# Kernel optimization log

Measured on AMD Instinct MI355X. Metric: run time of the kernel, lower is better.

Reference implementation:

```python
import jax, jax.numpy as jnp
import numpy as np

N = 8192
EMB = 256
KDIM = 32
AR = 1024
UTYPE = 233
TEMP = 0.8


def setup_inputs() -> dict:
    key = jax.random.key(0)
    ks = jax.random.split(key, 16)
    s = 0.05
    f32 = jnp.float32
    inp = {
        'utype_mask': jax.random.uniform(ks[0], (UTYPE,), f32),
        'entity_mask': jnp.ones((N,), f32),
        'entity_encodings': jax.random.normal(ks[1], (N, EMB), f32),
        'autoregressive_encoding': jax.random.normal(ks[2], (AR,), f32),
        # func_embed: Linear(233,256)+ReLU
        'W_fe': jax.random.normal(ks[3], (EMB, UTYPE), f32) * s, 'b_fe': jnp.zeros((EMB,), f32),
        # entity_keys: Conv1d(256,32,1) == pointwise linear
        'W_k': jax.random.normal(ks[4], (KDIM, EMB), f32) * s, 'b_k': jnp.zeros((KDIM,), f32),
        # argenc[0]: Linear(1024,256)
        'W_a0': jax.random.normal(ks[5], (EMB, AR), f32) * s, 'b_a0': jnp.zeros((EMB,), f32),
        # argenc[1]: ReLU -> Linear(256,32) -> ReLU
        'W_a1': jax.random.normal(ks[6], (KDIM, EMB), f32) * s, 'b_a1': jnp.zeros((KDIM,), f32),
        # LSTM(64,32) gates (forget, input-sigmoid, input-tanh, output) + shared LayerNorm(32)
        'W_f': jax.random.normal(ks[7], (KDIM, 2 * KDIM), f32) * s, 'b_f': jnp.zeros((KDIM,), f32),
        'W_i0': jax.random.normal(ks[8], (KDIM, 2 * KDIM), f32) * s, 'b_i0': jnp.zeros((KDIM,), f32),
        'W_i1': jax.random.normal(ks[9], (KDIM, 2 * KDIM), f32) * s, 'b_i1': jnp.zeros((KDIM,), f32),
        'W_o': jax.random.normal(ks[10], (KDIM, 2 * KDIM), f32) * s, 'b_o': jnp.zeros((KDIM,), f32),
        'ln_g': jnp.ones((KDIM,), f32), 'ln_b': jnp.zeros((KDIM,), f32),
        # argenc[3]: Linear(32,1024)+ReLU
        'W_a3': jax.random.normal(ks[11], (AR, KDIM), f32) * s, 'b_a3': jnp.zeros((AR,), f32),
        'self_unit_ct': 64,
    }
    return inp


def reference(utype_mask, entity_mask, entity_encodings, autoregressive_encoding,
              W_fe, b_fe, W_k, b_k, W_a0, b_a0, W_a1, b_a1,
              W_f, b_f, W_i0, b_i0, W_i1, b_i1, W_o, b_o, ln_g, ln_b,
              W_a3, b_a3, self_unit_ct):
    n = entity_encodings.shape[0]
    steps = min(64, int(self_unit_ct))

    def ln(x):  # shared LayerNorm(32), torch eps=1e-5, biased var
        m = x.mean()
        v = ((x - m) ** 2).mean()
        return (x - m) * jax.lax.rsqrt(v + 1e-5) * ln_g + ln_b

    def lstm(x, h):
        forget = ln(jax.nn.sigmoid(W_f @ x + b_f))
        remember = ln(jax.nn.sigmoid(W_i0 @ x + b_i0) * jnp.tanh(W_i1 @ x + b_i1))
        new_h = remember + forget * h
        out = jnp.tanh(new_h) * ln(jax.nn.sigmoid(W_o @ x + b_o))
        return out, new_h

    func_embed = jax.nn.relu(W_fe @ utype_mask + b_fe)          # (256,)
    keys = W_k @ entity_encodings.T + b_k[:, None]               # (32, N)

    def step(carry, _):
        q, h, mask, ar, sel, done = carry
        active = jnp.logical_not(done)
        i0 = W_a0 @ ar + b_a0 + func_embed                       # (256,)
        i1 = jax.nn.relu(W_a1 @ jax.nn.relu(i0) + b_a1)          # (32,)
        qn, hn = lstm(jnp.concatenate([i1, q]), h)
        sig = jax.nn.sigmoid(qn @ keys)                          # (N,)
        v = jnp.nan_to_num(jnp.exp(jnp.log(sig) / TEMP))
        ssum = v.sum()
        valid = ssum != 0
        soft = jnp.where(valid, v / jnp.where(valid, ssum, 1.0), 0.0)
        row = jnp.where(active & valid, soft, 0.0)
        pick = jnp.argmax(soft)                                  # deterministic stand-in for multinomial sample
        hit = active & valid & (mask[pick] != 0)
        selection = keys[:, pick]
        centered = selection - selection.mean()
        nan_free = jnp.logical_not(jnp.any(jnp.isnan(centered)))
        mask = jnp.where(hit, mask.at[pick].set(0.0), mask)
        sel = jnp.where(hit, sel.at[pick].set(1.0), sel)
        ar = jnp.where(hit & nan_free, ar + jax.nn.relu(W_a3 @ centered + b_a3), ar)
        done = done | (hit & jnp.logical_not(nan_free))          # emulates break
        q = jnp.where(active, qn, q)
        h = jnp.where(active, hn, h)
        return (q, h, mask, ar, sel, done), row

    init = (jnp.zeros((KDIM,), jnp.float32), jnp.zeros((KDIM,), jnp.float32),
            entity_mask, autoregressive_encoding,
            jnp.zeros((n,), jnp.float32), jnp.array(False))
    (_, _, _, ar_out, sel_out, _), rows = jax.lax.scan(step, init, None, length=steps)
    unit_logits = jnp.zeros((n, n), jnp.float32).at[:steps].set(rows)
    return unit_logits, sel_out, ar_out
```

## Files before the change

### kernel.cpp

```cpp
#include <hip/hip_runtime.h>
#include <math.h>


typedef float v4f __attribute__((ext_vector_type(4)));
typedef unsigned long long ull;

#define N_ENT 8192
#define EMB   256
#define KD    32
#define ARD   1024
#define UT    233
#define NSCAN 32
#define NZERO 224
#define NBLK  256

#define WS_KEYS 0
#define WS_C0   262144
#define WS_PAIR 262400
#define PR_RI0W  0
#define PR_CRI0  512
#define PR_CPART 577
#define PR_KMAX  641
#define PR_SACC  705
#define NPAIRS   737

struct Params {
  const float *um, *emask, *enc, *arin, *W_fe, *b_fe, *W_k, *b_k,
              *W_a0, *b_a0, *W_a1, *b_a1, *W_f, *b_f, *W_i0, *b_i0,
              *W_i1, *b_i1, *W_o, *b_o, *ln_g, *ln_b, *W_a3, *b_a3;
  const int* ct;
  float* out;
  float* wsf;
  int*   wsi;
};

__device__ __forceinline__ ull ld_pair(ull* p_) {
  return __hip_atomic_load(p_, __ATOMIC_RELAXED, __HIP_MEMORY_SCOPE_AGENT);
}
__device__ __forceinline__ void st_pair(ull* p_, ull v) {
  __hip_atomic_store(p_, v, __ATOMIC_RELAXED, __HIP_MEMORY_SCOPE_AGENT);
}
__device__ __forceinline__ void wait_ctr(ull* c, ull target) {
  int guard = 0;
  while (__hip_atomic_load(c, __ATOMIC_RELAXED, __HIP_MEMORY_SCOPE_AGENT) < target) {
    __builtin_amdgcn_s_sleep(1);
    if (++guard > (1 << 20)) break;
  }
}

__global__ __launch_bounds__(256) void k_init(Params p) {
  __shared__ float enc_s[32 * 260];
  __shared__ float um_s[UT];
  const int tid = threadIdx.x, bid = blockIdx.x;
  float* keys = p.wsf + WS_KEYS;

  if (bid == 0 && tid < UT) um_s[tid] = p.um[tid];
  if (bid == 3) {
    ull* pr = (ull*)(p.wsf + WS_PAIR);
    for (int i = tid; i < NPAIRS; i += 256) pr[i] = 0ull;
  }

  const int j0 = bid * 32;
  #pragma unroll
  for (int i = 0; i < 8; ++i) {
    int idx = i * 256 + tid;
    int row = idx >> 6, c4 = idx & 63;
    v4f v = *(const v4f*)(p.enc + (size_t)(j0 + row) * EMB + c4 * 4);
    *(v4f*)&enc_s[row * 260 + c4 * 4] = v;
  }
  __syncthreads();
  {
    const int jl = tid >> 3, kg = tid & 7;
    float acc[4];
    #pragma unroll
    for (int kk = 0; kk < 4; ++kk) acc[kk] = p.b_k[kg * 4 + kk];
    for (int e4 = 0; e4 < 64; ++e4) {
      v4f x = *(const v4f*)&enc_s[jl * 260 + e4 * 4];
      #pragma unroll
      for (int kk = 0; kk < 4; ++kk) {
        v4f w = *(const v4f*)(p.W_k + (size_t)(kg * 4 + kk) * EMB + e4 * 4);
        acc[kk] += x.x * w.x + x.y * w.y + x.z * w.z + x.w * w.w;
      }
    }
    const int j = j0 + jl;
    #pragma unroll
    for (int kk = 0; kk < 4; ++kk) keys[(size_t)(kg * 4 + kk) * N_ENT + j] = acc[kk];
  }
  if (bid == 0) {
    float a = p.b_fe[tid];
    const float* wr = p.W_fe + (size_t)tid * UT;
    for (int u = 0; u < UT; ++u) a += wr[u] * um_s[u];
    p.wsf[WS_C0 + tid] = fmaxf(a, 0.f) + p.b_a0[tid];
  }
}

__global__ __launch_bounds__(256, 1) void k_scan(Params p) {
  const int tid = threadIdx.x, bid = blockIdx.x;
  int ctv = p.ct[0];
  const int steps = ctv < 0 ? 0 : (ctv > 64 ? 64 : ctv);
  const size_t NN = (size_t)N_ENT * N_ENT;

  if (bid >= NSCAN) {
    v4f z = (v4f){0.f, 0.f, 0.f, 0.f};
    v4f* o4 = (v4f*)p.out;
    const size_t tot = NN / 4;
    for (size_t i = (size_t)steps * (N_ENT / 4) + (size_t)(bid - NSCAN) * 256 + tid;
         i < tot; i += (size_t)NZERO * 256)
      __builtin_nontemporal_store(z, o4 + i);
    return;
  }

  __shared__ float ar_s[32 * 33];
  __shared__ float ri0_s[8 * 33];
  __shared__ unsigned maskb[256], selb[256];
  __shared__ float x_i1[32], q_s[32], h_s[32], qnf[32];
  __shared__ float garr[128], fog[32], rem[32], og[32], cent[32];
  __shared__ float b_a1s[32], gb_s[128], lng_s[32], lnb_s[32], c0own[8];
  __shared__ float reds[4], rmaxs[4];
  __shared__ int   ridxs[4];
  __shared__ float ssum_s;
  __shared__ int   upd_s, done_s;

  ull*   pairb = (ull*)(p.wsf + WS_PAIR);
  ull*   ri0w  = pairb + PR_RI0W;
  ull*   cri0  = pairb + PR_CRI0;
  ull*   cpart = pairb + PR_CPART;
  ull*   kmaxp = pairb + PR_KMAX;
  float* saccp = (float*)(pairb + PR_SACC);
  const float* keys = p.wsf + WS_KEYS;

  for (int i = tid; i < ARD; i += 256) ar_s[(i >> 5) * 33 + (i & 31)] = p.arin[i];
  {
    unsigned mb = 0u;
    const float* em = p.emask + (size_t)tid * 32;
    #pragma unroll
    for (int j = 0; j < 32; ++j) mb |= (em[j] != 0.f) ? (1u << j) : 0u;
    maskb[tid] = mb; selb[tid] = 0u;
  }
  if (tid < 32) {
    b_a1s[tid] = p.b_a1[tid];
    lng_s[tid] = p.ln_g[tid]; lnb_s[tid] = p.ln_b[tid];
    q_s[tid] = 0.f; h_s[tid] = 0.f; qnf[tid] = 0.f; x_i1[tid] = 0.f;
  }
  if (tid < 128) {
    const int g = tid >> 5, r = tid & 31;
    const float* bg = (g == 0) ? p.b_f : (g == 1) ? p.b_i0 : (g == 2) ? p.b_i1 : p.b_o;
    gb_s[tid] = bg[r];
  }
  if (tid < 8) c0own[tid] = p.wsf[WS_C0 + bid * 8 + tid];
  if (tid == 0) done_s = 0;

  v4f w0[8];
  { const float* s = p.W_a0 + (size_t)(bid * 8 + (tid >> 5)) * ARD + (tid & 31) * 32;
    #pragma unroll
    for (int i = 0; i < 8; ++i) w0[i] = ((const v4f*)s)[i]; }
  v4f w1[8];
  { const float* s = p.W_a1 + (size_t)(tid >> 3) * EMB + (tid & 7) * 32;
    #pragma unroll
    for (int i = 0; i < 8; ++i) w1[i] = ((const v4f*)s)[i]; }
  v4f wg[8];
  { const int rowg = tid >> 1, g = rowg >> 5, r = rowg & 31, half = tid & 1;
    const float* W = (g == 0) ? p.W_f : (g == 1) ? p.W_i0 : (g == 2) ? p.W_i1 : p.W_o;
    const float* s = W + r * 64 + half * 32;
    #pragma unroll
    for (int i = 0; i < 8; ++i) wg[i] = ((const v4f*)s)[i]; }
  float kc[32];
  { const int gcol = bid * 256 + tid;
    #pragma unroll
    for (int k = 0; k < 32; ++k) kc[k] = keys[(size_t)k * N_ENT + gcol]; }
  __syncthreads();

  auto produce = [&](int tt) {
    const int seg = tid & 31, rl = tid >> 5;
    const float* a = &ar_s[seg * 33];
    float pa = 0.f;
    #pragma unroll
    for (int i = 0; i < 8; ++i) {
      v4f av = *(const v4f*)(a + 4 * i);
      pa += w0[i].x * av.x + w0[i].y * av.y + w0[i].z * av.z + w0[i].w * av.w;
    }
    #pragma unroll
    for (int m = 16; m; m >>= 1) pa += __shfl_xor(pa, m);
    if (seg == 0)
      st_pair(&ri0w[(tt & 1) * 256 + bid * 8 + rl],
              (ull)__float_as_uint(fmaxf(pa + c0own[rl], 0.f)));
  };
  produce(0);
  __syncthreads();
  if (tid == 0)
    __hip_atomic_fetch_add(&cri0[0], 1ull, __ATOMIC_RELAXED, __HIP_MEMORY_SCOPE_AGENT);

  float v_reg = 0.f;
  for (int t = 0; t < steps; ++t) {
    if (tid == 0) wait_ctr(&cri0[t], (ull)NSCAN);
    __syncthreads();
    {
      ull u = ld_pair(&ri0w[(t & 1) * 256 + tid]);
      ri0_s[(tid >> 5) * 33 + (tid & 31)] = __uint_as_float((unsigned)u);
    }
    __syncthreads();
    const int act = (done_s == 0);
    {
      const int r = tid >> 3, s8 = tid & 7;
      float p1 = 0.f;
      #pragma unroll
      for (int i = 0; i < 8; ++i) {
        const float* xx = &ri0_s[s8 * 33 + 4 * i];
        p1 += w1[i].x * xx[0] + w1[i].y * xx[1] + w1[i].z * xx[2] + w1[i].w * xx[3];
      }
      #pragma unroll
      for (int m = 4; m; m >>= 1) p1 += __shfl_xor(p1, m);
      if (s8 == 0) x_i1[r] = fmaxf(p1 + b_a1s[r], 0.f);
    }
    __syncthreads();
    {
      const int rowg = tid >> 1, g = rowg >> 5, half = tid & 1;
      const float* xsrc = half ? q_s : x_i1;
      float pg = 0.f;
      #pragma unroll
      for (int i = 0; i < 8; ++i)
        pg += wg[i].x * xsrc[4 * i] + wg[i].y * xsrc[4 * i + 1] +
              wg[i].z * xsrc[4 * i + 2] + wg[i].w * xsrc[4 * i + 3];
      pg += __shfl_xor(pg, 1);
      if (!half) {
        pg += gb_s[rowg];
        garr[rowg] = (g == 2) ? tanhf(pg) : 1.f / (1.f + __expf(-pg));
      }
    }
    __syncthreads();
    {
      const int w = tid >> 6, k = tid & 63;
      if (w < 3 && k < 32) {
        float a = (w == 0) ? garr[k] : (w == 1) ? garr[32 + k] * garr[64 + k] : garr[96 + k];
        float s = a;
        #pragma unroll
        for (int m = 16; m; m >>= 1) s += __shfl_xor(s, m);
        const float mean = s * (1.f / 32.f);
        const float d = a - mean;
        float vv = d * d;
        #pragma unroll
        for (int m = 16; m; m >>= 1) vv += __shfl_xor(vv, m);
        vv *= (1.f / 32.f);
        const float y = d * rsqrtf(vv + 1e-5f) * lng_s[k] + lnb_s[k];
        if (w == 0) fog[k] = y; else if (w == 1) rem[k] = y; else og[k] = y;
      }
    }
    __syncthreads();
    if (tid < 32) {
      const float nh = rem[tid] + fog[tid] * h_s[tid];
      const float qv = tanhf(nh) * og[tid];
      qnf[tid] = qv;
      if (act) { h_s[tid] = nh; q_s[tid] = qv; }
    }
    __syncthreads();

    {
      float dot = 0.f;
      #pragma unroll
      for (int k = 0; k < 32; ++k) dot += qnf[k] * kc[k];
      const float sig = 1.f / (1.f + __expf(-dot));
      const float v = __expf(__logf(sig) / 0.8f);
      v_reg = v;
      float sv = v, mv = v;
      int mi = (bid << 8) + tid;
      #pragma unroll
      for (int m = 32; m; m >>= 1) {
        sv += __shfl_xor(sv, m);
        const float ov = __shfl_xor(mv, m);
        const int oi = __shfl_xor(mi, m);
        if (ov > mv || (ov == mv && oi < mi)) { mv = ov; mi = oi; }
      }
      const int wv = tid >> 6;
      if ((tid & 63) == 0) { reds[wv] = sv; rmaxs[wv] = mv; ridxs[wv] = mi; }
    }
    __syncthreads();
    if (tid == 0) {
      float Sb = ((reds[0] + reds[1]) + reds[2]) + reds[3];
      float Mb = rmaxs[0]; int Ib = ridxs[0];
      #pragma unroll
      for (int i2 = 1; i2 < 4; ++i2)
        if (rmaxs[i2] > Mb || (rmaxs[i2] == Mb && ridxs[i2] < Ib)) { Mb = rmaxs[i2]; Ib = ridxs[i2]; }
      __hip_atomic_fetch_add(&saccp[t], Sb, __ATOMIC_RELAXED, __HIP_MEMORY_SCOPE_AGENT);
      const ull key = ((ull)__float_as_uint(Mb) << 32) | (ull)(0xFFFFFFFFu - (unsigned)Ib);
      __hip_atomic_fetch_max(&kmaxp[t], key, __ATOMIC_RELAXED, __HIP_MEMORY_SCOPE_AGENT);
      asm volatile("s_waitcnt vmcnt(0)" ::: "memory");
      __hip_atomic_fetch_add(&cpart[t], 1ull, __ATOMIC_RELAXED, __HIP_MEMORY_SCOPE_AGENT);
    }

    if (tid == 0) wait_ctr(&cpart[t], (ull)NSCAN);
    __syncthreads();
    if (tid < 32) {
      const float s = __hip_atomic_load(&saccp[t], __ATOMIC_RELAXED, __HIP_MEMORY_SCOPE_AGENT);
      const ull km = ld_pair(&kmaxp[t]);
      const int ii = (int)(0xFFFFFFFFu - (unsigned)(km & 0xFFFFFFFFull));
      const float kv = keys[(size_t)tid * N_ENT + ii];
      float mn = kv;
      #pragma unroll
      for (int mm = 16; mm; mm >>= 1) mn += __shfl_xor(mn, mm);
      mn *= (1.f / 32.f);
      const float cv = kv - mn;
      cent[tid] = cv;
      const unsigned long long bb = __ballot(cv != cv);
      if (tid == 0) {
        const int valid = (s != 0.f);
        const int nf = (bb == 0) ? 1 : 0;
        const unsigned mw = maskb[ii >> 5];
        const int hit = (act && valid && ((mw >> (ii & 31)) & 1)) ? 1 : 0;
        ssum_s = s;
        upd_s = (hit && nf) ? 1 : 0;
        if (hit) {
          maskb[ii >> 5] = mw & ~(1u << (ii & 31));
          selb[ii >> 5] |= (1u << (ii & 31));
          if (!nf) done_s = 1;
        }
      }
    }
    __syncthreads();
    {
      const float S = ssum_s;
      const float rowv = (act && (S != 0.f)) ? (v_reg / S) : 0.f;
      __builtin_nontemporal_store(rowv, p.out + (size_t)t * N_ENT + (bid << 8) + tid);
    }
    if (upd_s) {
      #pragma unroll
      for (int rr = 0; rr < 4; ++rr) {
        const int r = tid + rr * 256;
        const float* wr = p.W_a3 + (size_t)r * KD;
        float dl = p.b_a3[r];
        #pragma unroll
        for (int c4 = 0; c4 < 8; ++c4) {
          v4f wv4 = *(const v4f*)(wr + 4 * c4);
          dl += wv4.x * cent[4 * c4] + wv4.y * cent[4 * c4 + 1] +
                wv4.z * cent[4 * c4 + 2] + wv4.w * cent[4 * c4 + 3];
        }
        if (dl > 0.f) ar_s[(r >> 5) * 33 + (r & 31)] += dl;
      }
    }
    __syncthreads();
    produce(t + 1);
    __syncthreads();
    if (tid == 0)
      __hip_atomic_fetch_add(&cri0[t + 1], 1ull, __ATOMIC_RELAXED, __HIP_MEMORY_SCOPE_AGENT);
  }
  __syncthreads();

  if (bid == 0) {
    for (int i = tid; i < N_ENT; i += 256)
      p.out[NN + i] = ((selb[i >> 5] >> (i & 31)) & 1u) ? 1.f : 0.f;
  } else if (bid == 1) {
    for (int i = tid; i < ARD; i += 256)
      p.out[NN + N_ENT + i] = ar_s[(i >> 5) * 33 + (i & 31)];
  }
}

extern "C" void kernel_launch(void* const* d_in, const int* in_sizes, int n_in,
                              void* d_out, int out_size, void* d_ws, size_t ws_size,
                              hipStream_t stream) {
  (void)in_sizes; (void)n_in; (void)out_size; (void)ws_size;
  Params p;
  p.um    = (const float*)d_in[0];
  p.emask = (const float*)d_in[1];
  p.enc   = (const float*)d_in[2];
  p.arin  = (const float*)d_in[3];
  p.W_fe  = (const float*)d_in[4];
  p.b_fe  = (const float*)d_in[5];
  p.W_k   = (const float*)d_in[6];
  p.b_k   = (const float*)d_in[7];
  p.W_a0  = (const float*)d_in[8];
  p.b_a0  = (const float*)d_in[9];
  p.W_a1  = (const float*)d_in[10];
  p.b_a1  = (const float*)d_in[11];
  p.W_f   = (const float*)d_in[12];
  p.b_f   = (const float*)d_in[13];
  p.W_i0  = (const float*)d_in[14];
  p.b_i0  = (const float*)d_in[15];
  p.W_i1  = (const float*)d_in[16];
  p.b_i1  = (const float*)d_in[17];
  p.W_o   = (const float*)d_in[18];
  p.b_o   = (const float*)d_in[19];
  p.ln_g  = (const float*)d_in[20];
  p.ln_b  = (const float*)d_in[21];
  p.W_a3  = (const float*)d_in[22];
  p.b_a3  = (const float*)d_in[23];
  p.ct    = (const int*)d_in[24];
  p.out   = (float*)d_out;
  p.wsf   = (float*)d_ws;
  p.wsi   = (int*)d_ws;

  hipLaunchKernelGGL(k_init, dim3(NBLK), dim3(256), 0, stream, p);
  hipLaunchKernelGGL(k_scan, dim3(NBLK), dim3(256), 0, stream, p);
}
```

Baseline: 881.1 us.

## Shorten the per-step critical path with a single wavefront for AR update and produce

```diff
diff --git a/kernel.cpp b/kernel.cpp
--- a/kernel.cpp
+++ b/kernel.cpp
@@ -48,6 +48,10 @@
   }
 }
 
+__device__ __forceinline__ void bar_lds() {
+  asm volatile("s_waitcnt lgkmcnt(0)\n\ts_barrier" ::: "memory");
+}
+
 __global__ __launch_bounds__(256) void k_init(Params p) {
   __shared__ float enc_s[32 * 260];
   __shared__ float um_s[UT];
@@ -110,6 +114,7 @@
     return;
   }
 
+  __shared__ float wa0_lds[32 * 64 * 4];
   __shared__ float ar_s[32 * 33];
   __shared__ float ri0_s[8 * 33];
   __shared__ unsigned maskb[256], selb[256];
@@ -118,8 +123,7 @@
   __shared__ float b_a1s[32], gb_s[128], lng_s[32], lnb_s[32], c0own[8];
   __shared__ float reds[4], rmaxs[4];
   __shared__ int   ridxs[4];
-  __shared__ float ssum_s;
-  __shared__ int   upd_s, done_s;
+  __shared__ int   done_s;
 
   ull*   pairb = (ull*)(p.wsf + WS_PAIR);
   ull*   ri0w  = pairb + PR_RI0W;
@@ -130,6 +134,11 @@
   const float* keys = p.wsf + WS_KEYS;
 
   for (int i = tid; i < ARD; i += 256) ar_s[(i >> 5) * 33 + (i & 31)] = p.arin[i];
+  for (int e = tid; e < 8 * ARD; e += 256) {
+    const int r = e >> 10, c = e & 1023;
+    const int seg = c >> 7, rem2 = c & 127, i = rem2 >> 2, j = rem2 & 3;
+    wa0_lds[(i * 64 + seg * 8 + r) * 4 + j] = p.W_a0[(size_t)(bid * 8 + r) * ARD + c];
+  }
   {
     unsigned mb = 0u;
     const float* em = p.emask + (size_t)tid * 32;
@@ -150,10 +159,6 @@
   if (tid < 8) c0own[tid] = p.wsf[WS_C0 + bid * 8 + tid];
   if (tid == 0) done_s = 0;
 
-  v4f w0[8];
-  { const float* s = p.W_a0 + (size_t)(bid * 8 + (tid >> 5)) * ARD + (tid & 31) * 32;
-    #pragma unroll
-    for (int i = 0; i < 8; ++i) w0[i] = ((const v4f*)s)[i]; }
   v4f w1[8];
   { const float* s = p.W_a1 + (size_t)(tid >> 3) * EMB + (tid & 7) * 32;
     #pragma unroll
@@ -171,34 +176,37 @@
   __syncthreads();
 
   auto produce = [&](int tt) {
-    const int seg = tid & 31, rl = tid >> 5;
-    const float* a = &ar_s[seg * 33];
+    const int r = tid >> 3, seg = tid & 7;
     float pa = 0.f;
     #pragma unroll
-    for (int i = 0; i < 8; ++i) {
-      v4f av = *(const v4f*)(a + 4 * i);
-      pa += w0[i].x * av.x + w0[i].y * av.y + w0[i].z * av.z + w0[i].w * av.w;
-    }
-    #pragma unroll
-    for (int m = 16; m; m >>= 1) pa += __shfl_xor(pa, m);
+    for (int i = 0; i < 32; ++i) {
+      v4f wv = *(const v4f*)&wa0_lds[(i * 64 + seg * 8 + r) * 4];
+      const int c = seg * 128 + 4 * i;
+      const float* av = &ar_s[(c >> 5) * 33 + (c & 31)];
+      pa += wv.x * av[0] + wv.y * av[1] + wv.z * av[2] + wv.w * av[3];
+    }
+    pa += __shfl_xor(pa, 1);
+    pa += __shfl_xor(pa, 2);
+    pa += __shfl_xor(pa, 4);
     if (seg == 0)
-      st_pair(&ri0w[(tt & 1) * 256 + bid * 8 + rl],
-              (ull)__float_as_uint(fmaxf(pa + c0own[rl], 0.f)));
+      st_pair(&ri0w[(tt & 1) * 256 + bid * 8 + r],
+              (ull)__float_as_uint(fmaxf(pa + c0own[r], 0.f)));
   };
-  produce(0);
-  __syncthreads();
-  if (tid == 0)
-    __hip_atomic_fetch_add(&cri0[0], 1ull, __ATOMIC_RELAXED, __HIP_MEMORY_SCOPE_AGENT);
+  if (tid < 64) {
+    produce(0);
+    asm volatile("s_waitcnt vmcnt(0)" ::: "memory");
+    if (tid == 0)
+      __hip_atomic_fetch_add(&cri0[0], 1ull, __ATOMIC_RELAXED, __HIP_MEMORY_SCOPE_AGENT);
+  }
 
   float v_reg = 0.f;
   for (int t = 0; t < steps; ++t) {
-    if (tid == 0) wait_ctr(&cri0[t], (ull)NSCAN);
-    __syncthreads();
+    wait_ctr(&cri0[t], (ull)NSCAN);
     {
       ull u = ld_pair(&ri0w[(t & 1) * 256 + tid]);
       ri0_s[(tid >> 5) * 33 + (tid & 31)] = __uint_as_float((unsigned)u);
     }
-    __syncthreads();
+    bar_lds();
     const int act = (done_s == 0);
     {
       const int r = tid >> 3, s8 = tid & 7;
@@ -212,7 +220,7 @@
       for (int m = 4; m; m >>= 1) p1 += __shfl_xor(p1, m);
       if (s8 == 0) x_i1[r] = fmaxf(p1 + b_a1s[r], 0.f);
     }
-    __syncthreads();
+    bar_lds();
     {
       const int rowg = tid >> 1, g = rowg >> 5, half = tid & 1;
       const float* xsrc = half ? q_s : x_i1;
@@ -227,7 +235,7 @@
         garr[rowg] = (g == 2) ? tanhf(pg) : 1.f / (1.f + __expf(-pg));
       }
     }
-    __syncthreads();
+    bar_lds();
     {
       const int w = tid >> 6, k = tid & 63;
       if (w < 3 && k < 32) {
@@ -245,14 +253,14 @@
         if (w == 0) fog[k] = y; else if (w == 1) rem[k] = y; else og[k] = y;
       }
     }
-    __syncthreads();
+    bar_lds();
     if (tid < 32) {
       const float nh = rem[tid] + fog[tid] * h_s[tid];
       const float qv = tanhf(nh) * og[tid];
       qnf[tid] = qv;
       if (act) { h_s[tid] = nh; q_s[tid] = qv; }
     }
-    __syncthreads();
+    bar_lds();
 
     {
       float dot = 0.f;
@@ -273,7 +281,7 @@
       const int wv = tid >> 6;
       if ((tid & 63) == 0) { reds[wv] = sv; rmaxs[wv] = mv; ridxs[wv] = mi; }
     }
-    __syncthreads();
+    bar_lds();
     if (tid == 0) {
       float Sb = ((reds[0] + reds[1]) + reds[2]) + reds[3];
       float Mb = rmaxs[0]; int Ib = ridxs[0];
@@ -287,60 +295,61 @@
       __hip_atomic_fetch_add(&cpart[t], 1ull, __ATOMIC_RELAXED, __HIP_MEMORY_SCOPE_AGENT);
     }
 
-    if (tid == 0) wait_ctr(&cpart[t], (ull)NSCAN);
-    __syncthreads();
-    if (tid < 32) {
-      const float s = __hip_atomic_load(&saccp[t], __ATOMIC_RELAXED, __HIP_MEMORY_SCOPE_AGENT);
-      const ull km = ld_pair(&kmaxp[t]);
-      const int ii = (int)(0xFFFFFFFFu - (unsigned)(km & 0xFFFFFFFFull));
-      const float kv = keys[(size_t)tid * N_ENT + ii];
-      float mn = kv;
-      #pragma unroll
-      for (int mm = 16; mm; mm >>= 1) mn += __shfl_xor(mn, mm);
-      mn *= (1.f / 32.f);
-      const float cv = kv - mn;
-      cent[tid] = cv;
-      const unsigned long long bb = __ballot(cv != cv);
-      if (tid == 0) {
-        const int valid = (s != 0.f);
-        const int nf = (bb == 0) ? 1 : 0;
-        const unsigned mw = maskb[ii >> 5];
-        const int hit = (act && valid && ((mw >> (ii & 31)) & 1)) ? 1 : 0;
-        ssum_s = s;
-        upd_s = (hit && nf) ? 1 : 0;
-        if (hit) {
-          maskb[ii >> 5] = mw & ~(1u << (ii & 31));
-          selb[ii >> 5] |= (1u << (ii & 31));
-          if (!nf) done_s = 1;
+    wait_ctr(&cpart[t], (ull)NSCAN);
+    const float S = __hip_atomic_load(&saccp[t], __ATOMIC_RELAXED, __HIP_MEMORY_SCOPE_AGENT);
+    const ull km = ld_pair(&kmaxp[t]);
+    const int ii = (int)(0xFFFFFFFFu - (unsigned)(km & 0xFFFFFFFFull));
+    const int valid = (S != 0.f) ? 1 : 0;
+    const float rowv = (act && valid) ? (v_reg / S) : 0.f;
+    if (tid >= 64) {
+      __builtin_nontemporal_store(rowv, p.out + (size_t)t * N_ENT + (bid << 8) + tid);
+    } else {
+      if (tid < 32) {
+        const float kv = keys[(size_t)tid * N_ENT + ii];
+        float mn = kv;
+        #pragma unroll
+        for (int mm = 16; mm; mm >>= 1) mn += __shfl_xor(mn, mm);
+        mn *= (1.f / 32.f);
+        cent[tid] = kv - mn;
+      }
+      asm volatile("s_waitcnt lgkmcnt(0)" ::: "memory");
+      const unsigned mw = maskb[ii >> 5];
+      float cw[32]; int nanf = 0;
+      #pragma unroll
+      for (int g2 = 0; g2 < 8; ++g2) {
+        v4f x = *(const v4f*)&cent[4 * g2];
+        cw[4 * g2] = x.x; cw[4 * g2 + 1] = x.y; cw[4 * g2 + 2] = x.z; cw[4 * g2 + 3] = x.w;
+        nanf |= (x.x != x.x) | (x.y != x.y) | (x.z != x.z) | (x.w != x.w);
+      }
+      const int hit = (act && valid && ((mw >> (ii & 31)) & 1)) ? 1 : 0;
+      const int upd = (hit && !nanf) ? 1 : 0;
+      if (upd) {
+        #pragma unroll
+        for (int k = 0; k < 16; ++k) {
+          const int r = tid + 64 * k;
+          const float* wr = p.W_a3 + (size_t)r * KD;
+          float dl = p.b_a3[r];
+          #pragma unroll
+          for (int c4 = 0; c4 < 8; ++c4) {
+            v4f wv4 = *(const v4f*)(wr + 4 * c4);
+            dl += wv4.x * cw[4 * c4] + wv4.y * cw[4 * c4 + 1] +
+                  wv4.z * cw[4 * c4 + 2] + wv4.w * cw[4 * c4 + 3];
+          }
+          if (dl > 0.f) ar_s[(r >> 5) * 33 + (r & 31)] += dl;
         }
       }
-    }
-    __syncthreads();
-    {
-      const float S = ssum_s;
-      const float rowv = (act && (S != 0.f)) ? (v_reg / S) : 0.f;
+      if (tid == 0 && hit) {
+        maskb[ii >> 5] = mw & ~(1u << (ii & 31));
+        selb[ii >> 5] |= (1u << (ii & 31));
+        if (nanf) done_s = 1;
+      }
+      asm volatile("s_waitcnt lgkmcnt(0)" ::: "memory");
+      produce(t + 1);
+      asm volatile("s_waitcnt vmcnt(0)" ::: "memory");
+      if (tid == 0)
+        __hip_atomic_fetch_add(&cri0[t + 1], 1ull, __ATOMIC_RELAXED, __HIP_MEMORY_SCOPE_AGENT);
       __builtin_nontemporal_store(rowv, p.out + (size_t)t * N_ENT + (bid << 8) + tid);
     }
-    if (upd_s) {
-      #pragma unroll
-      for (int rr = 0; rr < 4; ++rr) {
-        const int r = tid + rr * 256;
-        const float* wr = p.W_a3 + (size_t)r * KD;
-        float dl = p.b_a3[r];
-        #pragma unroll
-        for (int c4 = 0; c4 < 8; ++c4) {
-          v4f wv4 = *(const v4f*)(wr + 4 * c4);
-          dl += wv4.x * cent[4 * c4] + wv4.y * cent[4 * c4 + 1] +
-                wv4.z * cent[4 * c4 + 2] + wv4.w * cent[4 * c4 + 3];
-        }
-        if (dl > 0.f) ar_s[(r >> 5) * 33 + (r & 31)] += dl;
-      }
-    }
-    __syncthreads();
-    produce(t + 1);
-    __syncthreads();
-    if (tid == 0)
-      __hip_atomic_fetch_add(&cri0[t + 1], 1ull, __ATOMIC_RELAXED, __HIP_MEMORY_SCOPE_AGENT);
   }
   __syncthreads();
 
```

Measured after the change: 1.025 ms. 16.3% more time.

## Recompute full W_a0 matvec redundantly per block to drop one grid barrier per step

Applied to the files above, without the earlier changes.

```diff
diff --git a/kernel.cpp b/kernel.cpp
--- a/kernel.cpp
+++ b/kernel.cpp
@@ -17,12 +17,10 @@
 #define WS_KEYS 0
 #define WS_C0   262144
 #define WS_PAIR 262400
-#define PR_RI0W  0
-#define PR_CRI0  512
-#define PR_CPART 577
-#define PR_KMAX  641
-#define PR_SACC  705
-#define NPAIRS   737
+#define PR_CPART 0
+#define PR_KMAX  64
+#define PR_SACC  128
+#define NPAIRS   160
 
 struct Params {
   const float *um, *emask, *enc, *arin, *W_fe, *b_fe, *W_k, *b_k,
@@ -37,9 +35,6 @@
 __device__ __forceinline__ ull ld_pair(ull* p_) {
   return __hip_atomic_load(p_, __ATOMIC_RELAXED, __HIP_MEMORY_SCOPE_AGENT);
 }
-__device__ __forceinline__ void st_pair(ull* p_, ull v) {
-  __hip_atomic_store(p_, v, __ATOMIC_RELAXED, __HIP_MEMORY_SCOPE_AGENT);
-}
 __device__ __forceinline__ void wait_ctr(ull* c, ull target) {
   int guard = 0;
   while (__hip_atomic_load(c, __ATOMIC_RELAXED, __HIP_MEMORY_SCOPE_AGENT) < target) {
@@ -112,24 +107,24 @@
 
   __shared__ float ar_s[32 * 33];
   __shared__ float ri0_s[8 * 33];
+  __shared__ float c0_s[256];
   __shared__ unsigned maskb[256], selb[256];
   __shared__ float x_i1[32], q_s[32], h_s[32], qnf[32];
   __shared__ float garr[128], fog[32], rem[32], og[32], cent[32];
-  __shared__ float b_a1s[32], gb_s[128], lng_s[32], lnb_s[32], c0own[8];
+  __shared__ float b_a1s[32], gb_s[128], lng_s[32], lnb_s[32];
   __shared__ float reds[4], rmaxs[4];
   __shared__ int   ridxs[4];
   __shared__ float ssum_s;
   __shared__ int   upd_s, done_s;
 
   ull*   pairb = (ull*)(p.wsf + WS_PAIR);
-  ull*   ri0w  = pairb + PR_RI0W;
-  ull*   cri0  = pairb + PR_CRI0;
   ull*   cpart = pairb + PR_CPART;
   ull*   kmaxp = pairb + PR_KMAX;
   float* saccp = (float*)(pairb + PR_SACC);
   const float* keys = p.wsf + WS_KEYS;
 
   for (int i = tid; i < ARD; i += 256) ar_s[(i >> 5) * 33 + (i & 31)] = p.arin[i];
+  c0_s[tid] = p.wsf[WS_C0 + tid];
   {
     unsigned mb = 0u;
     const float* em = p.emask + (size_t)tid * 32;
@@ -147,13 +142,8 @@
     const float* bg = (g == 0) ? p.b_f : (g == 1) ? p.b_i0 : (g == 2) ? p.b_i1 : p.b_o;
     gb_s[tid] = bg[r];
   }
-  if (tid < 8) c0own[tid] = p.wsf[WS_C0 + bid * 8 + tid];
   if (tid == 0) done_s = 0;
 
-  v4f w0[8];
-  { const float* s = p.W_a0 + (size_t)(bid * 8 + (tid >> 5)) * ARD + (tid & 31) * 32;
-    #pragma unroll
-    for (int i = 0; i < 8; ++i) w0[i] = ((const v4f*)s)[i]; }
   v4f w1[8];
   { const float* s = p.W_a1 + (size_t)(tid >> 3) * EMB + (tid & 7) * 32;
     #pragma unroll
@@ -170,36 +160,38 @@
     for (int k = 0; k < 32; ++k) kc[k] = keys[(size_t)k * N_ENT + gcol]; }
   __syncthreads();
 
-  auto produce = [&](int tt) {
-    const int seg = tid & 31, rl = tid >> 5;
-    const float* a = &ar_s[seg * 33];
-    float pa = 0.f;
-    #pragma unroll
-    for (int i = 0; i < 8; ++i) {
-      v4f av = *(const v4f*)(a + 4 * i);
-      pa += w0[i].x * av.x + w0[i].y * av.y + w0[i].z * av.z + w0[i].w * av.w;
-    }
-    #pragma unroll
-    for (int m = 16; m; m >>= 1) pa += __shfl_xor(pa, m);
-    if (seg == 0)
-      st_pair(&ri0w[(tt & 1) * 256 + bid * 8 + rl],
-              (ull)__float_as_uint(fmaxf(pa + c0own[rl], 0.f)));
+  auto recompute_ri0 = [&]() {
+    const int seg = tid & 7, r0 = tid >> 3;
+    v4f arseg[32];
+    #pragma unroll
+    for (int i = 0; i < 32; ++i) {
+      const int c = seg * 128 + 4 * i;
+      const float* a = &ar_s[(c >> 5) * 33 + (c & 31)];
+      arseg[i] = (v4f){a[0], a[1], a[2], a[3]};
+    }
+    #pragma unroll
+    for (int pass = 0; pass < 8; ++pass) {
+      const int r = r0 + 32 * pass;
+      const float* wrow = p.W_a0 + (size_t)r * ARD + seg * 128;
+      float pa = 0.f;
+      #pragma unroll
+      for (int i = 0; i < 32; ++i) {
+        v4f wv = ((const v4f*)wrow)[i];
+        pa += wv.x * arseg[i].x + wv.y * arseg[i].y + wv.z * arseg[i].z + wv.w * arseg[i].w;
+      }
+      pa += __shfl_xor(pa, 1);
+      pa += __shfl_xor(pa, 2);
+      pa += __shfl_xor(pa, 4);
+      if (seg == 0) ri0_s[(r >> 5) * 33 + (r & 31)] = fmaxf(pa + c0_s[r], 0.f);
+    }
   };
-  produce(0);
+  recompute_ri0();
   __syncthreads();
-  if (tid == 0)
-    __hip_atomic_fetch_add(&cri0[0], 1ull, __ATOMIC_RELAXED, __HIP_MEMORY_SCOPE_AGENT);
 
   float v_reg = 0.f;
   for (int t = 0; t < steps; ++t) {
-    if (tid == 0) wait_ctr(&cri0[t], (ull)NSCAN);
-    __syncthreads();
-    {
-      ull u = ld_pair(&ri0w[(t & 1) * 256 + tid]);
-      ri0_s[(tid >> 5) * 33 + (tid & 31)] = __uint_as_float((unsigned)u);
-    }
-    __syncthreads();
     const int act = (done_s == 0);
+
     {
       const int r = tid >> 3, s8 = tid & 7;
       float p1 = 0.f;
@@ -285,10 +277,10 @@
       __hip_atomic_fetch_max(&kmaxp[t], key, __ATOMIC_RELAXED, __HIP_MEMORY_SCOPE_AGENT);
       asm volatile("s_waitcnt vmcnt(0)" ::: "memory");
       __hip_atomic_fetch_add(&cpart[t], 1ull, __ATOMIC_RELAXED, __HIP_MEMORY_SCOPE_AGENT);
-    }
-
-    if (tid == 0) wait_ctr(&cpart[t], (ull)NSCAN);
-    __syncthreads();
+      wait_ctr(&cpart[t], (ull)NSCAN);
+    }
+    __syncthreads();
+
     if (tid < 32) {
       const float s = __hip_atomic_load(&saccp[t], __ATOMIC_RELAXED, __HIP_MEMORY_SCOPE_AGENT);
       const ull km = ld_pair(&kmaxp[t]);
@@ -337,10 +329,8 @@
       }
     }
     __syncthreads();
-    produce(t + 1);
-    __syncthreads();
-    if (tid == 0)
-      __hip_atomic_fetch_add(&cri0[t + 1], 1ull, __ATOMIC_RELAXED, __HIP_MEMORY_SCOPE_AGENT);
+    recompute_ri0();
+    __syncthreads();
   }
   __syncthreads();
 
```

Result: slower. 2.670 ms (+203.0%).

## Halve scan blocks so each handles 512 entities and 16 W_a0 rows

Applied to the files above, without the earlier changes.

```diff
diff --git a/kernel.cpp b/kernel.cpp
--- a/kernel.cpp
+++ b/kernel.cpp
@@ -10,8 +10,8 @@
 #define KD    32
 #define ARD   1024
 #define UT    233
-#define NSCAN 32
-#define NZERO 224
+#define NSCAN 16
+#define NZERO 240
 #define NBLK  256
 
 #define WS_KEYS 0
@@ -115,7 +115,7 @@
   __shared__ unsigned maskb[256], selb[256];
   __shared__ float x_i1[32], q_s[32], h_s[32], qnf[32];
   __shared__ float garr[128], fog[32], rem[32], og[32], cent[32];
-  __shared__ float b_a1s[32], gb_s[128], lng_s[32], lnb_s[32], c0own[8];
+  __shared__ float b_a1s[32], gb_s[128], lng_s[32], lnb_s[32], c0own[16];
   __shared__ float reds[4], rmaxs[4];
   __shared__ int   ridxs[4];
   __shared__ float ssum_s;
@@ -147,13 +147,13 @@
     const float* bg = (g == 0) ? p.b_f : (g == 1) ? p.b_i0 : (g == 2) ? p.b_i1 : p.b_o;
     gb_s[tid] = bg[r];
   }
-  if (tid < 8) c0own[tid] = p.wsf[WS_C0 + bid * 8 + tid];
+  if (tid < 16) c0own[tid] = p.wsf[WS_C0 + bid * 16 + tid];
   if (tid == 0) done_s = 0;
 
-  v4f w0[8];
-  { const float* s = p.W_a0 + (size_t)(bid * 8 + (tid >> 5)) * ARD + (tid & 31) * 32;
-    #pragma unroll
-    for (int i = 0; i < 8; ++i) w0[i] = ((const v4f*)s)[i]; }
+  v4f w0[16];
+  { const float* s = p.W_a0 + (size_t)(bid * 16 + (tid >> 4)) * ARD + (tid & 15) * 64;
+    #pragma unroll
+    for (int i = 0; i < 16; ++i) w0[i] = ((const v4f*)s)[i]; }
   v4f w1[8];
   { const float* s = p.W_a1 + (size_t)(tid >> 3) * EMB + (tid & 7) * 32;
     #pragma unroll
@@ -164,33 +164,38 @@
     const float* s = W + r * 64 + half * 32;
     #pragma unroll
     for (int i = 0; i < 8; ++i) wg[i] = ((const v4f*)s)[i]; }
-  float kc[32];
-  { const int gcol = bid * 256 + tid;
-    #pragma unroll
-    for (int k = 0; k < 32; ++k) kc[k] = keys[(size_t)k * N_ENT + gcol]; }
+  float kc0[32], kc1[32];
+  { const int g0 = bid * 512 + tid, g1 = g0 + 256;
+    #pragma unroll
+    for (int k = 0; k < 32; ++k) {
+      kc0[k] = keys[(size_t)k * N_ENT + g0];
+      kc1[k] = keys[(size_t)k * N_ENT + g1];
+    } }
   __syncthreads();
 
   auto produce = [&](int tt) {
-    const int seg = tid & 31, rl = tid >> 5;
-    const float* a = &ar_s[seg * 33];
+    const int r = tid >> 4, seg = tid & 15;
     float pa = 0.f;
     #pragma unroll
-    for (int i = 0; i < 8; ++i) {
-      v4f av = *(const v4f*)(a + 4 * i);
-      pa += w0[i].x * av.x + w0[i].y * av.y + w0[i].z * av.z + w0[i].w * av.w;
-    }
-    #pragma unroll
-    for (int m = 16; m; m >>= 1) pa += __shfl_xor(pa, m);
+    for (int i = 0; i < 16; ++i) {
+      const int c = seg * 64 + 4 * i;
+      const float* a = &ar_s[(c >> 5) * 33 + (c & 31)];
+      pa += w0[i].x * a[0] + w0[i].y * a[1] + w0[i].z * a[2] + w0[i].w * a[3];
+    }
+    pa += __shfl_xor(pa, 1);
+    pa += __shfl_xor(pa, 2);
+    pa += __shfl_xor(pa, 4);
+    pa += __shfl_xor(pa, 8);
     if (seg == 0)
-      st_pair(&ri0w[(tt & 1) * 256 + bid * 8 + rl],
-              (ull)__float_as_uint(fmaxf(pa + c0own[rl], 0.f)));
+      st_pair(&ri0w[(tt & 1) * 256 + bid * 16 + r],
+              (ull)__float_as_uint(fmaxf(pa + c0own[r], 0.f)));
   };
   produce(0);
   __syncthreads();
   if (tid == 0)
     __hip_atomic_fetch_add(&cri0[0], 1ull, __ATOMIC_RELAXED, __HIP_MEMORY_SCOPE_AGENT);
 
-  float v_reg = 0.f;
+  float v_reg0 = 0.f, v_reg1 = 0.f;
   for (int t = 0; t < steps; ++t) {
     if (tid == 0) wait_ctr(&cri0[t], (ull)NSCAN);
     __syncthreads();
@@ -255,14 +260,19 @@
     __syncthreads();
 
     {
-      float dot = 0.f;
-      #pragma unroll
-      for (int k = 0; k < 32; ++k) dot += qnf[k] * kc[k];
-      const float sig = 1.f / (1.f + __expf(-dot));
-      const float v = __expf(__logf(sig) / 0.8f);
-      v_reg = v;
-      float sv = v, mv = v;
-      int mi = (bid << 8) + tid;
+      float dot0 = 0.f, dot1 = 0.f;
+      #pragma unroll
+      for (int k = 0; k < 32; ++k) {
+        const float q = qnf[k];
+        dot0 += q * kc0[k];
+        dot1 += q * kc1[k];
+      }
+      const float v0 = __expf(__logf(1.f / (1.f + __expf(-dot0))) / 0.8f);
+      const float v1 = __expf(__logf(1.f / (1.f + __expf(-dot1))) / 0.8f);
+      v_reg0 = v0; v_reg1 = v1;
+      float sv = v0 + v1, mv = v0;
+      int mi = bid * 512 + tid;
+      if (v1 > v0) { mv = v1; mi += 256; }
       #pragma unroll
       for (int m = 32; m; m >>= 1) {
         sv += __shfl_xor(sv, m);
@@ -318,8 +328,10 @@
     __syncthreads();
     {
       const float S = ssum_s;
-      const float rowv = (act && (S != 0.f)) ? (v_reg / S) : 0.f;
-      __builtin_nontemporal_store(rowv, p.out + (size_t)t * N_ENT + (bid << 8) + tid);
+      const int av = (act && (S != 0.f)) ? 1 : 0;
+      float* orow = p.out + (size_t)t * N_ENT + bid * 512;
+      __builtin_nontemporal_store(av ? (v_reg0 / S) : 0.f, orow + tid);
+      __builtin_nontemporal_store(av ? (v_reg1 / S) : 0.f, orow + 256 + tid);
     }
     if (upd_s) {
       #pragma unroll
```

Measured after the change: 890.1 us. Within noise of the previous version (+1.0%).
